# Performance work log

Measured on AMD Instinct MI355X. Metric: run time of the kernel, lower is better.

## Reference

```python
import jax, jax.numpy as jnp
import numpy as np

DIM = 96          # channels (= groups for depthwise conv)
NUM_EXPERTS = 6
TOP_K = 3
B, H, W = 8, 192, 192


def _dwconv(x, w, b):
    # depthwise 3x3, stride 1, pad 1, groups = DIM (flag == 'C' branch)
    y = jax.lax.conv_general_dilated(
        x, w, window_strides=(1, 1), padding=((1, 1), (1, 1)),
        feature_group_count=DIM,
        dimension_numbers=('NCHW', 'OIHW', 'NCHW'))
    return y + b[None, :, None, None]


def _expert(x, w1, b1, w2, b2):
    return _dwconv(jax.nn.relu(_dwconv(x, w1, b1)), w2, b2)


def _gate(x, w_fc0, b_fc0, w_fc1, b_fc1):
    # AdaptiveMaxPool2d(1) + AdaptiveAvgPool2d(1), then flatten -> (B, DIM)
    pooled = jnp.max(x, axis=(2, 3)) + jnp.mean(x, axis=(2, 3))
    g = jax.nn.leaky_relu(pooled @ w_fc1.T + b_fc1, negative_slope=0.2)
    noise = jax.nn.softplus(pooled @ w_fc0.T + b_fc0)
    mu = jnp.mean(noise, axis=1, keepdims=True)
    sd = jnp.std(noise, axis=1, keepdims=True, ddof=1)  # torch.std is unbiased
    scores = g + (noise - mu) / sd
    _, idx = jax.lax.top_k(scores, TOP_K)  # (B, K)
    mask = jnp.any(jax.nn.one_hot(idx, NUM_EXPERTS, dtype=jnp.float32) > 0, axis=1)  # (B, E)
    # non-top-k logits of g set to -inf, softmax over experts
    return jax.nn.softmax(jnp.where(mask, g, -jnp.inf), axis=1)


def setup_inputs() -> dict:
    key = jax.random.key(0)
    ks = jax.random.split(key, 9)
    s = 0.05
    return {
        'x': jax.random.normal(ks[0], (B, DIM, H, W), jnp.float32),
        'w_fc0': jax.random.normal(ks[1], (NUM_EXPERTS, DIM), jnp.float32) * s,
        'b_fc0': jax.random.normal(ks[2], (NUM_EXPERTS,), jnp.float32) * s,
        'w_fc1': jax.random.normal(ks[3], (NUM_EXPERTS, DIM), jnp.float32) * s,
        'b_fc1': jax.random.normal(ks[4], (NUM_EXPERTS,), jnp.float32) * s,
        'ew1': jax.random.normal(ks[5], (NUM_EXPERTS, DIM, 1, 3, 3), jnp.float32) * s,
        'eb1': jax.random.normal(ks[6], (NUM_EXPERTS, DIM), jnp.float32) * s,
        'ew2': jax.random.normal(ks[7], (NUM_EXPERTS, DIM, 1, 3, 3), jnp.float32) * s,
        'eb2': jax.random.normal(ks[8], (NUM_EXPERTS, DIM), jnp.float32) * s,
    }


def reference(x, w_fc0, b_fc0, w_fc1, b_fc1, ew1, eb1, ew2, eb2):
    cof = _gate(x, w_fc0, b_fc0, w_fc1, b_fc1)  # (B, E), zero for non-top-k
    # Dense dispatch: experts with cof==0 contribute nothing, matching the
    # torch masked gather/scatter-accumulate loop exactly.
    outs = jax.vmap(lambda w1, b1, w2, b2: _expert(x, w1, b1, w2, b2))(
        ew1, eb1, ew2, eb2)  # (E, B, C, H, W)
    return jnp.einsum('ebchw,be->bchw', outs, cof)
```

## Files before the change

kernel.cpp:

```cpp
#include <hip/hip_runtime.h>
#include <math.h>

#define DIM 96
#define NE 6
#define NB 8
#define H 192
#define W 192
#define HW (H * W)
#define NQ 4
#define QF4 (HW / 4 / NQ)

typedef float f2 __attribute__((ext_vector_type(2)));

__global__ __launch_bounds__(256) void pool_partial(const float* __restrict__ x,
                                                    float* __restrict__ pmax,
                                                    float* __restrict__ psum) {
    int bc = blockIdx.x;
    int q = blockIdx.y;
    const float4* xp = (const float4*)(x + (size_t)bc * HW) + q * QF4;
    int tid = threadIdx.x;
    float vmax = -INFINITY, vsum = 0.f;
    for (int i = tid; i < QF4; i += 256) {
        float4 v = xp[i];
        vmax = fmaxf(vmax, fmaxf(fmaxf(v.x, v.y), fmaxf(v.z, v.w)));
        vsum += v.x + v.y + v.z + v.w;
    }
    for (int off = 32; off; off >>= 1) {
        vmax = fmaxf(vmax, __shfl_down(vmax, off, 64));
        vsum += __shfl_down(vsum, off, 64);
    }
    __shared__ float smax[4], ssum[4];
    if ((tid & 63) == 0) { smax[tid >> 6] = vmax; ssum[tid >> 6] = vsum; }
    __syncthreads();
    if (tid == 0) {
        float m = smax[0], s = ssum[0];
        for (int w = 1; w < 4; ++w) { m = fmaxf(m, smax[w]); s += ssum[w]; }
        pmax[q * (NB * DIM) + bc] = m;
        psum[q * (NB * DIM) + bc] = s;
    }
}

__global__ __launch_bounds__(128) void gate_kernel(const float* __restrict__ pmax,
                                                   const float* __restrict__ psum,
                                                   const float* __restrict__ w_fc0,
                                                   const float* __restrict__ b_fc0,
                                                   const float* __restrict__ w_fc1,
                                                   const float* __restrict__ b_fc1,
                                                   float* __restrict__ cof) {
    __shared__ float sp[NB * DIM];
    __shared__ float sw1[NE * DIM], sw0[NE * DIM];
    __shared__ float z1s[NB * NE], z0s[NB * NE];
    int tid = threadIdx.x;
    for (int i = tid; i < NB * DIM; i += 128) {
        float m = pmax[i], s = psum[i];
        for (int q = 1; q < NQ; ++q) {
            m = fmaxf(m, pmax[q * (NB * DIM) + i]);
            s += psum[q * (NB * DIM) + i];
        }
        sp[i] = m + s * (1.0f / (float)HW);
    }
    for (int i = tid; i < NE * DIM; i += 128) {
        sw1[i] = w_fc1[i];
        sw0[i] = w_fc0[i];
    }
    __syncthreads();
    if (tid < 2 * NB * NE) {
        int pair = (tid < NB * NE) ? tid : tid - NB * NE;
        int b = pair / NE, e = pair - b * NE;
        const float* wp = ((tid < NB * NE) ? sw1 : sw0) + e * DIM;
        float z = (tid < NB * NE) ? b_fc1[e] : b_fc0[e];
        const float* pp = sp + b * DIM;
        for (int i = 0; i < DIM; ++i) z = fmaf(pp[i], wp[i], z);
        if (tid < NB * NE) z1s[pair] = z; else z0s[pair] = z;
    }
    __syncthreads();
    if (tid < NB) {
        int b = tid;
        float g[NE], noise[NE];
        for (int e = 0; e < NE; ++e) {
            float z1 = z1s[b * NE + e], z0 = z0s[b * NE + e];
            g[e] = (z1 > 0.f) ? z1 : 0.2f * z1;
            noise[e] = (z0 > 20.f) ? z0 : log1pf(expf(z0));
        }
        float mu = 0.f;
        for (int e = 0; e < NE; ++e) mu += noise[e];
        mu *= (1.0f / NE);
        float var = 0.f;
        for (int e = 0; e < NE; ++e) { float d = noise[e] - mu; var += d * d; }
        var *= (1.0f / (NE - 1));
        float sd = sqrtf(var);
        float scores[NE];
        for (int e = 0; e < NE; ++e) scores[e] = g[e] + (noise[e] - mu) / sd;
        bool chosen[NE] = {false, false, false, false, false, false};
        for (int k = 0; k < 3; ++k) {
            float best = -INFINITY; int bi = 0;
            for (int e = 0; e < NE; ++e)
                if (!chosen[e] && scores[e] > best) { best = scores[e]; bi = e; }
            chosen[bi] = true;
        }
        float m = -INFINITY;
        for (int e = 0; e < NE; ++e) if (chosen[e]) m = fmaxf(m, g[e]);
        float s = 0.f;
        for (int e = 0; e < NE; ++e) if (chosen[e]) s += expf(g[e] - m);
        float inv = 1.0f / s;
        for (int e = 0; e < NE; ++e)
            cof[b * NE + e] = chosen[e] ? expf(g[e] - m) * inv : 0.f;
    }
}

#define TY 32
#define RPW 8
#define SW 200
#define XROWS (TY + 4)

__device__ __forceinline__ f2 splat2(float v) { f2 r; r.x = v; r.y = v; return r; }

__device__ __forceinline__ float c3(const float* Wt, float bb,
                                    const float* A, const float* B,
                                    const float* Cc, int o) {
    float s = fmaf(Wt[2], A[o + 2], bb);
    s = fmaf(Wt[1], A[o + 1], s);
    s = fmaf(Wt[0], A[o], s);
    s = fmaf(Wt[5], B[o + 2], s);
    s = fmaf(Wt[4], B[o + 1], s);
    s = fmaf(Wt[3], B[o], s);
    s = fmaf(Wt[8], Cc[o + 2], s);
    s = fmaf(Wt[7], Cc[o + 1], s);
    s = fmaf(Wt[6], Cc[o], s);
    return s;
}

__device__ __forceinline__ f2 c3p(const f2* Wt, f2 bb,
                                  const float* A, const float* B,
                                  const float* Cc, int o) {
    f2 s = __builtin_elementwise_fma(Wt[2], splat2(A[o + 2]), bb);
    s = __builtin_elementwise_fma(Wt[1], splat2(A[o + 1]), s);
    s = __builtin_elementwise_fma(Wt[0], splat2(A[o]), s);
    s = __builtin_elementwise_fma(Wt[5], splat2(B[o + 2]), s);
    s = __builtin_elementwise_fma(Wt[4], splat2(B[o + 1]), s);
    s = __builtin_elementwise_fma(Wt[3], splat2(B[o]), s);
    s = __builtin_elementwise_fma(Wt[8], splat2(Cc[o + 2]), s);
    s = __builtin_elementwise_fma(Wt[7], splat2(Cc[o + 1]), s);
    s = __builtin_elementwise_fma(Wt[6], splat2(Cc[o]), s);
    return s;
}

__device__ __forceinline__ f2 c3q(const f2* Wt, f2 bb,
                                  const f2* A, const f2* B,
                                  const f2* Cc, int o) {
    f2 s = __builtin_elementwise_fma(Wt[2], A[o + 2], bb);
    s = __builtin_elementwise_fma(Wt[1], A[o + 1], s);
    s = __builtin_elementwise_fma(Wt[0], A[o], s);
    s = __builtin_elementwise_fma(Wt[5], B[o + 2], s);
    s = __builtin_elementwise_fma(Wt[4], B[o + 1], s);
    s = __builtin_elementwise_fma(Wt[3], B[o], s);
    s = __builtin_elementwise_fma(Wt[8], Cc[o + 2], s);
    s = __builtin_elementwise_fma(Wt[7], Cc[o + 1], s);
    s = __builtin_elementwise_fma(Wt[6], Cc[o], s);
    return s;
}

__global__ __launch_bounds__(256, 3) void moe_kernel(const float* __restrict__ x,
                                                     const float* __restrict__ ew1,
                                                     const float* __restrict__ eb1,
                                                     const float* __restrict__ ew2,
                                                     const float* __restrict__ eb2,
                                                     const float* __restrict__ cof,
                                                     float* __restrict__ out) {
    __shared__ float xs[XROWS * SW];
    const int sb = blockIdx.x;
    const int c = blockIdx.y;
    const int b = blockIdx.z;
    const int ty0 = sb * TY;
    const int tid = threadIdx.x;
    const int lane = tid & 63;
    const int wv = tid >> 6;

    if (tid < 2 * XROWS) {
        int r = tid >> 1;
        int side = tid & 1;
        *(float4*)&xs[r * SW + side * 196] = make_float4(0.f, 0.f, 0.f, 0.f);
    }

    const float* xp = x + ((size_t)(b * DIM + c)) * HW;
    #pragma unroll
    for (int it = 0; it < 7; ++it) {
        int f = tid + it * 256;
        if (f < XROWS * 48) {
            int r = f / 48;
            int k = f - r * 48;
            int gh = ty0 + r - 2;
            float4 v = make_float4(0.f, 0.f, 0.f, 0.f);
            if (gh >= 0 && gh < H) v = *(const float4*)(xp + (size_t)gh * W + k * 4);
            *(float4*)&xs[r * SW + 4 + k * 4] = v;
        }
    }

    const float* cofb = cof + b * NE;
    int e0 = 0, e1 = 0, e2 = 0;
    float q0 = 0.f, q1 = 0.f, q2 = 0.f;
    int n = 0;
    #pragma unroll
    for (int e = 0; e < NE; ++e) {
        float ce = cofb[e];
        if (ce != 0.f) {
            if (n == 0)      { e0 = e; q0 = ce; }
            else if (n == 1) { e1 = e; q1 = ce; }
            else if (n == 2) { e2 = e; q2 = ce; }
            ++n;
        }
    }
    e0 = __builtin_amdgcn_readfirstlane(e0);
    e1 = __builtin_amdgcn_readfirstlane(e1);
    e2 = __builtin_amdgcn_readfirstlane(e2);
    q0 = __int_as_float(__builtin_amdgcn_readfirstlane(__float_as_int(q0)));
    q1 = __int_as_float(__builtin_amdgcn_readfirstlane(__float_as_int(q1)));
    q2 = __int_as_float(__builtin_amdgcn_readfirstlane(__float_as_int(q2)));

    f2 W1p[9], W2p[9];
    float W1s[9], W2s[9];
    {
        const float* p10 = ew1 + (size_t)(e0 * DIM + c) * 9;
        const float* p11 = ew1 + (size_t)(e1 * DIM + c) * 9;
        const float* p12 = ew1 + (size_t)(e2 * DIM + c) * 9;
        const float* p20 = ew2 + (size_t)(e0 * DIM + c) * 9;
        const float* p21 = ew2 + (size_t)(e1 * DIM + c) * 9;
        const float* p22 = ew2 + (size_t)(e2 * DIM + c) * 9;
        #pragma unroll
        for (int k = 0; k < 9; ++k) {
            W1p[k].x = p10[k]; W1p[k].y = p11[k]; W1s[k] = p12[k];
            W2p[k].x = p20[k]; W2p[k].y = p21[k]; W2s[k] = p22[k];
        }
    }
    f2 B1p, B2p;
    B1p.x = eb1[e0 * DIM + c]; B1p.y = eb1[e1 * DIM + c];
    B2p.x = eb2[e0 * DIM + c]; B2p.y = eb2[e1 * DIM + c];
    const float B1s = eb1[e2 * DIM + c];
    const float B2s = eb2[e2 * DIM + c];
    const float CE0 = q0, CE1 = q1, CE2 = q2;

    __syncthreads();

    const int r0 = ty0 + wv * RPW;
    const int lbase = (wv * RPW) * SW + 3 * lane + 3;
    const bool l0 = (lane == 0);
    const bool l63 = (lane == 63);

    float X[3][5];
    f2 Yp[3][5];
    float Ysc[3][5];
    #pragma unroll
    for (int k = 0; k < 5; ++k) X[0][k] = xs[lbase + k];
    #pragma unroll
    for (int k = 0; k < 5; ++k) X[1][k] = xs[lbase + SW + k];

    float* op = out + ((size_t)(b * DIM + c)) * HW + (size_t)r0 * W + 3 * lane;
    const f2 zero2 = splat2(0.f);

    #pragma unroll
    for (int j = 0; j < RPW + 2; ++j) {
        float* xN = X[(j + 2) % 3];
        #pragma unroll
        for (int k = 0; k < 5; ++k) xN[k] = xs[lbase + (j + 2) * SW + k];
        const float* xA = X[j % 3];
        const float* xB = X[(j + 1) % 3];
        const float* xC = xN;

        f2 y0p = c3p(W1p, B1p, xA, xB, xC, 0);
        f2 y1p = c3p(W1p, B1p, xA, xB, xC, 1);
        f2 y2p = c3p(W1p, B1p, xA, xB, xC, 2);
        float y0s = c3(W1s, B1s, xA, xB, xC, 0);
        float y1s = c3(W1s, B1s, xA, xB, xC, 1);
        float y2s = c3(W1s, B1s, xA, xB, xC, 2);
        y0p = __builtin_elementwise_max(y0p, zero2);
        y1p = __builtin_elementwise_max(y1p, zero2);
        y2p = __builtin_elementwise_max(y2p, zero2);
        y0s = fmaxf(y0s, 0.f); y1s = fmaxf(y1s, 0.f); y2s = fmaxf(y2s, 0.f);
        if (j == 0 || j == RPW + 1) {
            int ry = r0 - 1 + j;
            if (ry < 0 || ry >= H) {
                y0p = zero2; y1p = zero2; y2p = zero2;
                y0s = 0.f; y1s = 0.f; y2s = 0.f;
            }
        }
        float ylpx = __shfl_up(y2p.x, 1), ylpy = __shfl_up(y2p.y, 1);
        float yls = __shfl_up(y2s, 1);
        float yrpx = __shfl_down(y0p.x, 1), yrpy = __shfl_down(y0p.y, 1);
        float yrs = __shfl_down(y0s, 1);
        if (l0)  { ylpx = 0.f; ylpy = 0.f; yls = 0.f; }
        if (l63) { yrpx = 0.f; yrpy = 0.f; yrs = 0.f; }
        f2* ywp = Yp[j % 3];
        float* yws = Ysc[j % 3];
        ywp[0].x = ylpx; ywp[0].y = ylpy;
        ywp[1] = y0p; ywp[2] = y1p; ywp[3] = y2p;
        ywp[4].x = yrpx; ywp[4].y = yrpy;
        yws[0] = yls; yws[1] = y0s; yws[2] = y1s; yws[3] = y2s; yws[4] = yrs;

        if (j >= 2) {
            const f2* pA = Yp[(j + 1) % 3];
            const f2* pB = Yp[(j + 2) % 3];
            const f2* pC = ywp;
            const float* sA = Ysc[(j + 1) % 3];
            const float* sB = Ysc[(j + 2) % 3];
            const float* sC = yws;
            f2 s0p = c3q(W2p, B2p, pA, pB, pC, 0);
            f2 s1p = c3q(W2p, B2p, pA, pB, pC, 1);
            f2 s2p = c3q(W2p, B2p, pA, pB, pC, 2);
            float s0s = c3(W2s, B2s, sA, sB, sC, 0);
            float s1s = c3(W2s, B2s, sA, sB, sC, 1);
            float s2s = c3(W2s, B2s, sA, sB, sC, 2);
            float a0 = fmaf(CE2, s0s, fmaf(CE1, s0p.y, fmaf(CE0, s0p.x, 0.f)));
            float a1 = fmaf(CE2, s1s, fmaf(CE1, s1p.y, fmaf(CE0, s1p.x, 0.f)));
            float a2 = fmaf(CE2, s2s, fmaf(CE1, s2p.y, fmaf(CE0, s2p.x, 0.f)));
            op[0] = a0; op[1] = a1; op[2] = a2;
            op += W;
        }
    }
}

extern "C" void kernel_launch(void* const* d_in, const int* in_sizes, int n_in,
                              void* d_out, int out_size, void* d_ws, size_t ws_size,
                              hipStream_t stream) {
    const float* x     = (const float*)d_in[0];
    const float* w_fc0 = (const float*)d_in[1];
    const float* b_fc0 = (const float*)d_in[2];
    const float* w_fc1 = (const float*)d_in[3];
    const float* b_fc1 = (const float*)d_in[4];
    const float* ew1   = (const float*)d_in[5];
    const float* eb1   = (const float*)d_in[6];
    const float* ew2   = (const float*)d_in[7];
    const float* eb2   = (const float*)d_in[8];
    float* out = (float*)d_out;

    float* pmax = (float*)d_ws;
    float* psum = pmax + NQ * NB * DIM;
    float* cof  = psum + NQ * NB * DIM;

    dim3 pg(NB * DIM, NQ);
    pool_partial<<<pg, 256, 0, stream>>>(x, pmax, psum);
    gate_kernel<<<1, 128, 0, stream>>>(pmax, psum, w_fc0, b_fc0, w_fc1, b_fc1, cof);
    dim3 grid(H / TY, DIM, NB);
    moe_kernel<<<grid, 256, 0, stream>>>(x, ew1, eb1, ew2, eb2, cof, out);
}
```

Measured before the change: 257.3 us.

## Load input rows directly from global memory into registers, drop LDS staging

Removes the shared-memory tile of input rows and the block-wide barrier. Each lane now loads its own five-element row window straight from global memory into a 4-deep register ring, prefetching one row ahead, with the edge lanes clamping their offsets and zeroing halo values. This cuts LDS traffic, the cooperative fill and the __syncthreads. In exchange it issues scalar, uncoalesced, overlapping global loads that depend on L1/L2 hits, and uses more registers for the extra ring slot.

New measurement: 261.1 us. About the same (+1.5%).

```diff
diff --git a/kernel.cpp b/kernel.cpp
--- a/kernel.cpp
+++ b/kernel.cpp
@@ -110,8 +110,6 @@
 
 #define TY 32
 #define RPW 8
-#define SW 200
-#define XROWS (TY + 4)
 
 __device__ __forceinline__ f2 splat2(float v) { f2 r; r.x = v; r.y = v; return r; }
 
@@ -160,6 +158,25 @@
     return s;
 }
 
+#define LOADROW(xr, dst) do {                                         \
+    int _r = (xr);                                                    \
+    if (_r >= 0 && _r < H) {                                          \
+        const float* _q = xl + (size_t)_r * W;                        \
+        float _v0 = _q[offm1];                                        \
+        float _v1 = _q[0];                                            \
+        float _v2 = _q[1];                                            \
+        float _v3 = _q[2];                                            \
+        float _v4 = _q[off3];                                         \
+        if (l0)  _v0 = 0.f;                                           \
+        if (l63) _v4 = 0.f;                                           \
+        (dst)[0] = _v0; (dst)[1] = _v1; (dst)[2] = _v2;               \
+        (dst)[3] = _v3; (dst)[4] = _v4;                               \
+    } else {                                                          \
+        (dst)[0] = 0.f; (dst)[1] = 0.f; (dst)[2] = 0.f;               \
+        (dst)[3] = 0.f; (dst)[4] = 0.f;                               \
+    }                                                                 \
+} while (0)
+
 __global__ __launch_bounds__(256, 3) void moe_kernel(const float* __restrict__ x,
                                                      const float* __restrict__ ew1,
                                                      const float* __restrict__ eb1,
@@ -167,7 +184,6 @@
                                                      const float* __restrict__ eb2,
                                                      const float* __restrict__ cof,
                                                      float* __restrict__ out) {
-    __shared__ float xs[XROWS * SW];
     const int sb = blockIdx.x;
     const int c = blockIdx.y;
     const int b = blockIdx.z;
@@ -175,26 +191,8 @@
     const int tid = threadIdx.x;
     const int lane = tid & 63;
     const int wv = tid >> 6;
-
-    if (tid < 2 * XROWS) {
-        int r = tid >> 1;
-        int side = tid & 1;
-        *(float4*)&xs[r * SW + side * 196] = make_float4(0.f, 0.f, 0.f, 0.f);
-    }
-
-    const float* xp = x + ((size_t)(b * DIM + c)) * HW;
-    #pragma unroll
-    for (int it = 0; it < 7; ++it) {
-        int f = tid + it * 256;
-        if (f < XROWS * 48) {
-            int r = f / 48;
-            int k = f - r * 48;
-            int gh = ty0 + r - 2;
-            float4 v = make_float4(0.f, 0.f, 0.f, 0.f);
-            if (gh >= 0 && gh < H) v = *(const float4*)(xp + (size_t)gh * W + k * 4);
-            *(float4*)&xs[r * SW + 4 + k * 4] = v;
-        }
-    }
+    const bool l0 = (lane == 0);
+    const bool l63 = (lane == 63);
 
     const float* cofb = cof + b * NE;
     int e0 = 0, e1 = 0, e2 = 0;
@@ -239,32 +237,28 @@
     const float B2s = eb2[e2 * DIM + c];
     const float CE0 = q0, CE1 = q1, CE2 = q2;
 
-    __syncthreads();
-
     const int r0 = ty0 + wv * RPW;
-    const int lbase = (wv * RPW) * SW + 3 * lane + 3;
-    const bool l0 = (lane == 0);
-    const bool l63 = (lane == 63);
-
-    float X[3][5];
+    const float* xl = x + ((size_t)(b * DIM + c)) * HW + 3 * lane;
+    const int offm1 = l0 ? 0 : -1;
+    const int off3  = l63 ? 2 : 3;
+
+    float X[4][5];
     f2 Yp[3][5];
     float Ysc[3][5];
-    #pragma unroll
-    for (int k = 0; k < 5; ++k) X[0][k] = xs[lbase + k];
-    #pragma unroll
-    for (int k = 0; k < 5; ++k) X[1][k] = xs[lbase + SW + k];
+    LOADROW(r0 - 2, X[0]);
+    LOADROW(r0 - 1, X[1]);
+    LOADROW(r0,     X[2]);
 
     float* op = out + ((size_t)(b * DIM + c)) * HW + (size_t)r0 * W + 3 * lane;
     const f2 zero2 = splat2(0.f);
 
     #pragma unroll
     for (int j = 0; j < RPW + 2; ++j) {
-        float* xN = X[(j + 2) % 3];
-        #pragma unroll
-        for (int k = 0; k < 5; ++k) xN[k] = xs[lbase + (j + 2) * SW + k];
-        const float* xA = X[j % 3];
-        const float* xB = X[(j + 1) % 3];
-        const float* xC = xN;
+        if (j <= RPW)
+            LOADROW(r0 + j + 1, X[(j + 3) & 3]);
+        const float* xA = X[j & 3];
+        const float* xB = X[(j + 1) & 3];
+        const float* xC = X[(j + 2) & 3];
 
         f2 y0p = c3p(W1p, B1p, xA, xB, xC, 0);
         f2 y1p = c3p(W1p, B1p, xA, xB, xC, 1);
```
